# Kernel optimization log

Measured on AMD Instinct MI355X. Metric: run time of the kernel, lower is better.

Reference implementation:

```python
import jax, jax.numpy as jnp
import numpy as np

B, V, T, S, C, NH, H, MULT = 1, 2, 2, 16384, 128, 9, 4, 2
DH = C // H


def _ln(x, g, b):
    m = jnp.mean(x, -1, keepdims=True)
    v = jnp.mean((x - m) ** 2, -1, keepdims=True)
    return (x - m) * jax.lax.rsqrt(v + 1e-5) * g + b


def setup_inputs():
    key = jax.random.key(0)
    ks = jax.random.split(key, 16)
    sc = 0.02
    return {
        "x": jax.random.normal(ks[0], (B, V, T, S, C), jnp.float32),
        "adjc": jax.random.randint(ks[1], (S, NH), 0, S, dtype=jnp.int32),
        "mask": jax.random.bernoulli(ks[2], 0.1, (B, V, T, S)),
        "ln1_g": jnp.ones((C,), jnp.float32),
        "ln1_b": jnp.zeros((C,), jnp.float32),
        "Wq": sc * jax.random.normal(ks[3], (C, C), jnp.float32),
        "Wkv": sc * jax.random.normal(ks[4], (C, 2 * C), jnp.float32),
        "b_kv": jnp.zeros((2 * C,), jnp.float32),
        "W_nh": sc * jax.random.normal(ks[5], (NH, NH), jnp.float32),
        "W_ao": sc * jax.random.normal(ks[6], (C, C), jnp.float32),
        "ln2_g": jnp.ones((C,), jnp.float32),
        "ln2_b": jnp.zeros((C,), jnp.float32),
        "W1": sc * jax.random.normal(ks[7], (C, MULT * C), jnp.float32),
        "b1": jnp.zeros((MULT * C,), jnp.float32),
        "W2": sc * jax.random.normal(ks[8], (MULT * C, C), jnp.float32),
        "b2": jnp.zeros((C,), jnp.float32),
        "gamma": 0.1 * jnp.ones((C,), jnp.float32),
        "Wout": sc * jax.random.normal(ks[9], (C, C), jnp.float32),
    }


def reference(x, adjc, mask, ln1_g, ln1_b, Wq, Wkv, b_kv, W_nh, W_ao,
              ln2_g, ln2_b, W1, b1, W2, b2, gamma, Wout):
    # 1. per-zoom embedding layer (LayerNorm, identity linear)
    xe = _ln(x, ln1_g, ln1_b)  # [b,v,t,s,c]
    # 2. query projection, q_len = 1 per grid cell
    q = jnp.einsum("bvtsc,cd->bvtsd", xe, Wq)
    # 3. neighborhood gather (grid_layer.get_nh) + fused KV projection
    kv_nh = xe[:, :, :, adjc, :]                       # [b,v,t,s,nh,c]
    kv = jnp.einsum("bvtsnc,cd->bvtsnd", kv_nh, Wkv) + b_kv  # [b,v,t,s,nh,2c]
    # factorized nh-mixing with residual skip (skip_dims=[True,...])
    kv = kv + jnp.einsum("bvtsnd,nm->bvtsmd", kv, W_nh)
    # 4. gathered neighbor mask (True = masked out)
    m_nh = mask[:, :, :, adjc]                          # [b,v,t,s,nh]
    # 5. multi-head cross attention, q_len=1, kv_len=nh
    k, v = jnp.split(kv, 2, axis=-1)                    # each [b,v,t,s,nh,c]
    qh = q.reshape(B, V, T, S, H, DH)
    kh = k.reshape(B, V, T, S, NH, H, DH)
    vh = v.reshape(B, V, T, S, NH, H, DH)
    scores = jnp.einsum("bvtshd,bvtsnhd->bvtshn", qh, kh) / jnp.sqrt(
        jnp.asarray(DH, qh.dtype))
    scores = jnp.where(m_nh[:, :, :, :, None, :], -1e9, scores)
    attn = jax.nn.softmax(scores, axis=-1)
    o = jnp.einsum("bvtshn,bvtsnhd->bvtshd", attn, vh).reshape(B, V, T, S, C)
    o = jnp.einsum("bvtsc,cd->bvtsd", o, W_ao)
    # 6. residual insert
    x = x + o
    # 7. MLP block with layer-scale gamma
    xm = _ln(x, ln2_g, ln2_b)
    h = jax.nn.gelu(jnp.einsum("bvtsc,cd->bvtsd", xm, W1) + b1)
    x = x + gamma * (jnp.einsum("bvtsd,dc->bvtsc", h, W2) + b2)
    # 8. output layer
    return jnp.einsum("bvtsc,cd->bvtsd", x, Wout)
```

## Files before the change

### kernel.cpp

```cpp
#include <hip/hip_runtime.h>
#include <math.h>

namespace {

typedef float f32x4 __attribute__((ext_vector_type(4)));
typedef short s16x8 __attribute__((ext_vector_type(8)));

constexpr int C_   = 128;
constexpr int S_   = 16384;
constexpr int NTOK = 65536;

__device__ __forceinline__ unsigned short f2bf(float f) {
    unsigned int u = __float_as_uint(f);
    unsigned int r = (u + 0x7FFFu + ((u >> 16) & 1u)) >> 16;
    return (unsigned short)r;
}
__device__ __forceinline__ float bf2f(unsigned short h) {
    return __uint_as_float(((unsigned int)h) << 16);
}
__device__ __forceinline__ float gelu_tanh(float v) {
    const float k0 = 0.7978845608028654f;
    float u = k0 * (v + 0.044715f * v * v * v);
    float au = fabsf(u);
    float E = __expf(2.0f * au);
    float th = 1.0f - 2.0f / (1.0f + E);
    th = (u < 0.f) ? -th : th;
    return 0.5f * v * (1.0f + th);
}

__global__ __launch_bounds__(256) void prep_weights(
    const float* __restrict__ Wq, const float* __restrict__ Wkv,
    const float* __restrict__ W_ao, const float* __restrict__ W1,
    const float* __restrict__ W2, const float* __restrict__ Wout,
    unsigned short* __restrict__ Wf)
{
    int idx = blockIdx.x * 256 + threadIdx.x;
    if (idx >= 147456) return;
    int seg, off, K, N; const float* src = nullptr;
    if (idx < 49152)       { seg = 0; off = 0;      K = 128; N = 384; }
    else if (idx < 65536)  { seg = 1; off = 49152;  K = 128; N = 128; src = W_ao; }
    else if (idx < 98304)  { seg = 2; off = 65536;  K = 128; N = 256; src = W1; }
    else if (idx < 131072) { seg = 3; off = 98304;  K = 256; N = 128; src = W2; }
    else                   { seg = 4; off = 131072; K = 128; N = 128; src = Wout; }
    int local = idx - off;
    int j    = local & 7;
    int lane = (local >> 3) & 63;
    int tl   = local >> 9;
    int KB   = K >> 5;
    int kb   = tl % KB;
    int nt   = tl / KB;
    int k    = kb * 32 + ((lane >> 4) << 3) + j;
    int col  = (nt << 4) + (lane & 15);
    float v;
    if (seg == 0) v = (col < 128) ? Wq[k * 128 + col] : Wkv[k * 256 + (col - 128)];
    else          v = src[k * N + col];
    Wf[idx] = f2bf(v);
}

__global__ __launch_bounds__(256, 2) void qkv_kernel(
    const float* __restrict__ x,
    const float* __restrict__ ln1_g, const float* __restrict__ ln1_b,
    const unsigned short* __restrict__ Wf,
    const float* __restrict__ b_kv,
    float* qout, unsigned short* __restrict__ kout,
    unsigned short* __restrict__ vout)
{
    __shared__ unsigned short xet[64 * 128];
    const int tile = blockIdx.x;
    const int t = threadIdx.x;

    {
        const int row = t >> 2;
        const int q4  = t & 3;
        const int tok = tile * 64 + row;
        const float* xr = x + (size_t)tok * C_ + q4 * 32;
        float v[32];
        float s0 = 0.f, s1 = 0.f;
        #pragma unroll
        for (int i = 0; i < 32; i += 4) {
            float4 f = *(const float4*)(xr + i);
            v[i] = f.x; v[i+1] = f.y; v[i+2] = f.z; v[i+3] = f.w;
            s0 += f.x + f.y + f.z + f.w;
            s1 += f.x*f.x + f.y*f.y + f.z*f.z + f.w*f.w;
        }
        s0 += __shfl_xor(s0, 1, 64); s1 += __shfl_xor(s1, 1, 64);
        s0 += __shfl_xor(s0, 2, 64); s1 += __shfl_xor(s1, 2, 64);
        const float mean = s0 * (1.0f / C_);
        const float var  = s1 * (1.0f / C_) - mean * mean;
        const float inv  = rsqrtf(var + 1e-5f);
        #pragma unroll
        for (int jj = 0; jj < 4; ++jj) {
            unsigned short tmp[8];
            #pragma unroll
            for (int j = 0; j < 8; ++j) {
                int k = q4 * 32 + jj * 8 + j;
                tmp[j] = f2bf((v[jj*8 + j] - mean) * inv * ln1_g[k] + ln1_b[k]);
            }
            int byte = row * 256 + (q4 * 32 + jj * 8) * 2;
            byte ^= (row & 7) << 4;
            *(s16x8*)((char*)xet + byte) = *(const s16x8*)tmp;
        }
    }
    __syncthreads();

    const int w = t >> 6, l = t & 63;
    const int arow = (w << 4) + (l & 15);
    s16x8 af[4];
    #pragma unroll
    for (int kb = 0; kb < 4; ++kb) {
        int byte = arow * 256 + (kb * 32 + ((l >> 4) << 3)) * 2;
        byte ^= (arow & 7) << 4;
        af[kb] = *(const s16x8*)((const char*)xet + byte);
    }
    f32x4 acc[24];
    #pragma unroll
    for (int nt = 0; nt < 24; ++nt) acc[nt] = (f32x4){0.f, 0.f, 0.f, 0.f};
    #pragma unroll
    for (int nt = 0; nt < 24; ++nt) {
        #pragma unroll
        for (int kb = 0; kb < 4; ++kb) {
            s16x8 bf = *(const s16x8*)(Wf + (size_t)((nt * 4 + kb) * 64 + l) * 8);
            acc[nt] = __builtin_amdgcn_mfma_f32_16x16x32_bf16(af[kb], bf, acc[nt], 0, 0, 0);
        }
    }
    const int r0 = (l >> 4) << 2;
    const int colb = l & 15;
    #pragma unroll
    for (int nt = 0; nt < 8; ++nt) {
        const int col = nt * 16 + colb;
        #pragma unroll
        for (int reg = 0; reg < 4; ++reg) {
            const size_t tokr = (size_t)tile * 64 + (w << 4) + r0 + reg;
            qout[tokr * 128 + col] = acc[nt][reg];
        }
    }
    #pragma unroll
    for (int i = 0; i < 8; ++i) {
        const int ch = i * 16 + colb;
        const float bk = b_kv[ch];
        const float bv = b_kv[ch + 128];
        #pragma unroll
        for (int reg = 0; reg < 4; ++reg) {
            const size_t tokr = (size_t)tile * 64 + (w << 4) + r0 + reg;
            kout[tokr * 128 + ch] = f2bf(acc[8 + i][reg] + bk);
            vout[tokr * 128 + ch] = f2bf(acc[16 + i][reg] + bv);
        }
    }
}

__global__ __launch_bounds__(256, 5) void attn_kernel(
    const int* __restrict__ adjc, const unsigned char* __restrict__ mask,
    const float* __restrict__ wnh,
    const float* __restrict__ qbuf,
    const unsigned short* __restrict__ kbuf,
    const unsigned short* __restrict__ vbuf,
    unsigned short* __restrict__ obuf)
{
    __shared__ unsigned int sidx[32][9];

    const int d   = blockIdx.x;
    const int xcd = d & 7, dj = d >> 3;
    const int bid = (xcd >> 1) * 512 + dj * 2 + (xcd & 1);
    const size_t base = (size_t)bid * 32;
    const int s0  = (int)(base & (S_ - 1));
    const int bvt = (int)(base >> 14);
    const int t = threadIdx.x;

    for (int i = t; i < 288; i += 256) {
        int r = i / 9, n = i - r * 9;
        int nb = adjc[(s0 + r) * 9 + n];
        unsigned int gi = (unsigned int)(bvt * S_ + nb);
        sidx[r][n] = gi | (mask[gi] ? 0x80000000u : 0u);
    }
    __syncthreads();

    const int w = t >> 6, l = t & 63;
    const int g = l >> 3, j = l & 7;
    const int r = w * 8 + g;
    const size_t tok = base + r;

    float q[16];
    {
        const float4* qp = (const float4*)(qbuf + tok * 128 + j * 16);
        #pragma unroll
        for (int i = 0; i < 4; ++i) {
            float4 f = qp[i];
            q[4*i] = f.x; q[4*i+1] = f.y; q[4*i+2] = f.z; q[4*i+3] = f.w;
        }
    }
    unsigned int gm[9];
    #pragma unroll
    for (int n = 0; n < 9; ++n) gm[n] = sidx[r][n];

    float sp[9];
    #pragma unroll
    for (int n = 0; n < 9; ++n) {
        const s16x8* kp = (const s16x8*)(kbuf +
            (size_t)(gm[n] & 0x7fffffffu) * 128 + j * 16);
        s16x8 k0 = kp[0], k1 = kp[1];
        float a = 0.f;
        #pragma unroll
        for (int i = 0; i < 8; ++i) a += q[i]     * bf2f((unsigned short)k0[i]);
        #pragma unroll
        for (int i = 0; i < 8; ++i) a += q[8 + i] * bf2f((unsigned short)k1[i]);
        sp[n] = a;
    }
    #pragma unroll
    for (int n = 0; n < 9; ++n) sp[n] += __shfl_xor(sp[n], 1, 64);

    float S[9];
    #pragma unroll
    for (int m = 0; m < 9; ++m) {
        float a = sp[m];
        #pragma unroll
        for (int n = 0; n < 9; ++n) a += sp[n] * wnh[n * 9 + m];
        a *= 0.17677669529663687f;
        S[m] = (gm[m] & 0x80000000u) ? -1e9f : a;
    }
    float mx = S[0];
    #pragma unroll
    for (int m = 1; m < 9; ++m) mx = fmaxf(mx, S[m]);
    float e[9], se = 0.f;
    #pragma unroll
    for (int m = 0; m < 9; ++m) { e[m] = __expf(S[m] - mx); se += e[m]; }
    const float inv = 1.f / se;

    float ap[9];
    #pragma unroll
    for (int n = 0; n < 9; ++n) {
        float a = e[n];
        #pragma unroll
        for (int m = 0; m < 9; ++m) a += wnh[n * 9 + m] * e[m];
        ap[n] = a * inv;
    }

    float o[16];
    #pragma unroll
    for (int i = 0; i < 16; ++i) o[i] = 0.f;
    #pragma unroll
    for (int n = 0; n < 9; ++n) {
        const s16x8* vp = (const s16x8*)(vbuf +
            (size_t)(gm[n] & 0x7fffffffu) * 128 + j * 16);
        s16x8 v0 = vp[0], v1 = vp[1];
        const float a = ap[n];
        #pragma unroll
        for (int i = 0; i < 8; ++i) o[i]     += a * bf2f((unsigned short)v0[i]);
        #pragma unroll
        for (int i = 0; i < 8; ++i) o[8 + i] += a * bf2f((unsigned short)v1[i]);
    }
    unsigned short tmp[16];
    #pragma unroll
    for (int i = 0; i < 16; ++i) tmp[i] = f2bf(o[i]);
    s16x8* op = (s16x8*)(obuf + tok * 256 + j * 16);
    op[0] = *(const s16x8*)tmp;
    op[1] = *(const s16x8*)(tmp + 8);
}

__global__ __launch_bounds__(256, 2) void mlp_kernel(
    const float* __restrict__ x,
    const unsigned short* obuf,
    const unsigned short* __restrict__ Wao_f, const unsigned short* __restrict__ W1f,
    const unsigned short* __restrict__ W2f, const unsigned short* __restrict__ Woutf,
    const float* __restrict__ ln2_g, const float* __restrict__ ln2_b,
    const float* __restrict__ b1, const float* __restrict__ b2,
    const float* __restrict__ gamma,
    float* outp)
{
    __shared__ unsigned short act[8192];
    __shared__ float sred[2][32][2];
    const int tile = blockIdx.x;
    const int t = threadIdx.x;
    const int w = t >> 6, l = t & 63;
    const int wr = w >> 1, wc = w & 1;
    const int arow = (wr << 4) + (l & 15);
    const int crow0 = (wr << 4) + ((l >> 4) << 2);
    const int colb = l & 15;
    const size_t base = (size_t)tile * 32;

    s16x8 af[4];
    #pragma unroll
    for (int kb = 0; kb < 4; ++kb)
        af[kb] = *(const s16x8*)(obuf + (base + arow) * 256 + kb * 32 + ((l >> 4) << 3));
    f32x4 acc1[4];
    #pragma unroll
    for (int nt = 0; nt < 4; ++nt) acc1[nt] = (f32x4){0.f, 0.f, 0.f, 0.f};
    #pragma unroll
    for (int nt = 0; nt < 4; ++nt) {
        const int ntg = wc * 4 + nt;
        #pragma unroll
        for (int kb = 0; kb < 4; ++kb) {
            s16x8 bf = *(const s16x8*)(Wao_f + (size_t)((ntg * 4 + kb) * 64 + l) * 8);
            acc1[nt] = __builtin_amdgcn_mfma_f32_16x16x32_bf16(af[kb], bf, acc1[nt], 0, 0, 0);
        }
    }

    float x1v[4][4];
    float ss[4] = {0.f, 0.f, 0.f, 0.f}, s2[4] = {0.f, 0.f, 0.f, 0.f};
    #pragma unroll
    for (int nt = 0; nt < 4; ++nt) {
        const int col = wc * 64 + nt * 16 + colb;
        #pragma unroll
        for (int reg = 0; reg < 4; ++reg) {
            const size_t tokr = base + crow0 + reg;
            float xv = x[tokr * 128 + col] + acc1[nt][reg];
            x1v[nt][reg] = xv;
            ss[reg] += xv;
            s2[reg] += xv * xv;
        }
    }
    #pragma unroll
    for (int off = 1; off < 16; off <<= 1) {
        #pragma unroll
        for (int reg = 0; reg < 4; ++reg) {
            ss[reg] += __shfl_xor(ss[reg], off, 64);
            s2[reg] += __shfl_xor(s2[reg], off, 64);
        }
    }
    if (colb == 0) {
        #pragma unroll
        for (int reg = 0; reg < 4; ++reg) {
            sred[wc][crow0 + reg][0] = ss[reg];
            sred[wc][crow0 + reg][1] = s2[reg];
        }
    }
    __syncthreads();
    float mean[4], inv[4];
    #pragma unroll
    for (int reg = 0; reg < 4; ++reg) {
        const int row = crow0 + reg;
        float sum = sred[0][row][0] + sred[1][row][0];
        float sq  = sred[0][row][1] + sred[1][row][1];
        mean[reg] = sum * (1.0f / 128.f);
        float var = sq * (1.0f / 128.f) - mean[reg] * mean[reg];
        inv[reg] = rsqrtf(var + 1e-5f);
    }
    #pragma unroll
    for (int nt = 0; nt < 4; ++nt) {
        const int col = wc * 64 + nt * 16 + colb;
        const float lg = ln2_g[col], lb = ln2_b[col];
        #pragma unroll
        for (int reg = 0; reg < 4; ++reg) {
            const int lrow = crow0 + reg;
            float xm = (x1v[nt][reg] - mean[reg]) * inv[reg] * lg + lb;
            int byte = lrow * 256 + col * 2;
            byte ^= (lrow & 7) << 4;
            *(unsigned short*)((char*)act + byte) = f2bf(xm);
        }
    }
    __syncthreads();

    #pragma unroll
    for (int kb = 0; kb < 4; ++kb) {
        int byte = arow * 256 + (kb * 32 + ((l >> 4) << 3)) * 2;
        byte ^= (arow & 7) << 4;
        af[kb] = *(const s16x8*)((const char*)act + byte);
    }
    f32x4 acc2[8];
    #pragma unroll
    for (int nt = 0; nt < 8; ++nt) acc2[nt] = (f32x4){0.f, 0.f, 0.f, 0.f};
    #pragma unroll
    for (int nt = 0; nt < 8; ++nt) {
        const int ntg = wc * 8 + nt;
        #pragma unroll
        for (int kb = 0; kb < 4; ++kb) {
            s16x8 bf = *(const s16x8*)(W1f + (size_t)((ntg * 4 + kb) * 64 + l) * 8);
            acc2[nt] = __builtin_amdgcn_mfma_f32_16x16x32_bf16(af[kb], bf, acc2[nt], 0, 0, 0);
        }
    }
    __syncthreads();
    #pragma unroll
    for (int nt = 0; nt < 8; ++nt) {
        const int col2 = wc * 128 + nt * 16 + colb;
        const float bb = b1[col2];
        #pragma unroll
        for (int reg = 0; reg < 4; ++reg) {
            const int lrow = crow0 + reg;
            float hv = gelu_tanh(acc2[nt][reg] + bb);
            int byte = lrow * 512 + col2 * 2;
            byte ^= (lrow & 7) << 4;
            *(unsigned short*)((char*)act + byte) = f2bf(hv);
        }
    }
    __syncthreads();

    f32x4 acc3[4];
    #pragma unroll
    for (int nt = 0; nt < 4; ++nt) acc3[nt] = (f32x4){0.f, 0.f, 0.f, 0.f};
    #pragma unroll
    for (int kb = 0; kb < 8; ++kb) {
        int byte = arow * 512 + (kb * 32 + ((l >> 4) << 3)) * 2;
        byte ^= (arow & 7) << 4;
        s16x8 hf = *(const s16x8*)((const char*)act + byte);
        #pragma unroll
        for (int nt = 0; nt < 4; ++nt) {
            const int ntg = wc * 4 + nt;
            s16x8 bf = *(const s16x8*)(W2f + (size_t)((ntg * 8 + kb) * 64 + l) * 8);
            acc3[nt] = __builtin_amdgcn_mfma_f32_16x16x32_bf16(hf, bf, acc3[nt], 0, 0, 0);
        }
    }
    __syncthreads();
    #pragma unroll
    for (int nt = 0; nt < 4; ++nt) {
        const int col = wc * 64 + nt * 16 + colb;
        const float gm = gamma[col], bb = b2[col];
        #pragma unroll
        for (int reg = 0; reg < 4; ++reg) {
            const int lrow = crow0 + reg;
            float y = x1v[nt][reg] + gm * (acc3[nt][reg] + bb);
            int byte = lrow * 256 + col * 2;
            byte ^= (lrow & 7) << 4;
            *(unsigned short*)((char*)act + byte) = f2bf(y);
        }
    }
    __syncthreads();

    #pragma unroll
    for (int kb = 0; kb < 4; ++kb) {
        int byte = arow * 256 + (kb * 32 + ((l >> 4) << 3)) * 2;
        byte ^= (arow & 7) << 4;
        af[kb] = *(const s16x8*)((const char*)act + byte);
    }
    f32x4 acc4[4];
    #pragma unroll
    for (int nt = 0; nt < 4; ++nt) acc4[nt] = (f32x4){0.f, 0.f, 0.f, 0.f};
    #pragma unroll
    for (int nt = 0; nt < 4; ++nt) {
        const int ntg = wc * 4 + nt;
        #pragma unroll
        for (int kb = 0; kb < 4; ++kb) {
            s16x8 bf = *(const s16x8*)(Woutf + (size_t)((ntg * 4 + kb) * 64 + l) * 8);
            acc4[nt] = __builtin_amdgcn_mfma_f32_16x16x32_bf16(af[kb], bf, acc4[nt], 0, 0, 0);
        }
    }
    #pragma unroll
    for (int nt = 0; nt < 4; ++nt) {
        const int col = wc * 64 + nt * 16 + colb;
        #pragma unroll
        for (int reg = 0; reg < 4; ++reg) {
            const size_t tokr = base + crow0 + reg;
            outp[tokr * 128 + col] = acc4[nt][reg];
        }
    }
}

}

extern "C" void kernel_launch(void* const* d_in, const int* in_sizes, int n_in,
                              void* d_out, int out_size, void* d_ws, size_t ws_size,
                              hipStream_t stream) {
    const float* x     = (const float*)d_in[0];
    const int*   adjc  = (const int*)d_in[1];
    const unsigned char* mask = (const unsigned char*)d_in[2];
    const float* ln1_g = (const float*)d_in[3];
    const float* ln1_b = (const float*)d_in[4];
    const float* Wq    = (const float*)d_in[5];
    const float* Wkv   = (const float*)d_in[6];
    const float* b_kv  = (const float*)d_in[7];
    const float* W_nh  = (const float*)d_in[8];
    const float* W_ao  = (const float*)d_in[9];
    const float* ln2_g = (const float*)d_in[10];
    const float* ln2_b = (const float*)d_in[11];
    const float* W1    = (const float*)d_in[12];
    const float* b1    = (const float*)d_in[13];
    const float* W2    = (const float*)d_in[14];
    const float* b2    = (const float*)d_in[15];
    const float* gamma = (const float*)d_in[16];
    const float* Wout  = (const float*)d_in[17];

    unsigned short* kbuf = (unsigned short*)d_ws;
    unsigned short* vbuf = kbuf + (size_t)NTOK * 128;
    unsigned short* Wf   = vbuf + (size_t)NTOK * 128;
    unsigned short* Wao_f  = Wf + 49152;
    unsigned short* W1f    = Wf + 65536;
    unsigned short* W2f    = Wf + 98304;
    unsigned short* Woutf  = Wf + 131072;

    float*          qbuf = (float*)d_out;
    unsigned short* obuf = (unsigned short*)d_out;

    prep_weights<<<576, 256, 0, stream>>>(Wq, Wkv, W_ao, W1, W2, Wout, Wf);
    qkv_kernel<<<NTOK / 64, 256, 0, stream>>>(x, ln1_g, ln1_b, Wf, b_kv,
                                              qbuf, kbuf, vbuf);
    attn_kernel<<<NTOK / 32, 256, 0, stream>>>(adjc, mask, W_nh,
                                               qbuf, kbuf, vbuf, obuf);
    mlp_kernel<<<NTOK / 32, 256, 0, stream>>>(x, obuf, Wao_f, W1f, W2f, Woutf,
                                              ln2_g, ln2_b, b1, b2, gamma,
                                              (float*)d_out);
}
```

Baseline: 157.8 us.

## Fuse neighborhood attention into MLP kernel via shared-memory handoff

Merges the attention kernel and the MLP kernel into one launch. Each block first computes the gathered-neighbor attention output for its 32 tokens and writes it in bf16 to a swizzled LDS tile. The Wao/MLP stage then reads its MFMA operands from that tile instead of a global intermediate buffer. This removes the global write and re-read of the attention output and one kernel launch. In exchange, the latency-bound gather phase now runs at the MLP kernel's lower occupancy bound (2 blocks instead of 5), and an extra barrier is needed before the LDS tile is reused.

Result: faster. 134.2 us (-15.0%).

```diff
diff --git a/kernel.cpp b/kernel.cpp
--- a/kernel.cpp
+++ b/kernel.cpp
@@ -148,117 +148,13 @@
     }
 }
 
-__global__ __launch_bounds__(256, 5) void attn_kernel(
+__global__ __launch_bounds__(256, 2) void attn_mlp_kernel(
+    const float* __restrict__ x,
     const int* __restrict__ adjc, const unsigned char* __restrict__ mask,
     const float* __restrict__ wnh,
     const float* __restrict__ qbuf,
     const unsigned short* __restrict__ kbuf,
     const unsigned short* __restrict__ vbuf,
-    unsigned short* __restrict__ obuf)
-{
-    __shared__ unsigned int sidx[32][9];
-
-    const int d   = blockIdx.x;
-    const int xcd = d & 7, dj = d >> 3;
-    const int bid = (xcd >> 1) * 512 + dj * 2 + (xcd & 1);
-    const size_t base = (size_t)bid * 32;
-    const int s0  = (int)(base & (S_ - 1));
-    const int bvt = (int)(base >> 14);
-    const int t = threadIdx.x;
-
-    for (int i = t; i < 288; i += 256) {
-        int r = i / 9, n = i - r * 9;
-        int nb = adjc[(s0 + r) * 9 + n];
-        unsigned int gi = (unsigned int)(bvt * S_ + nb);
-        sidx[r][n] = gi | (mask[gi] ? 0x80000000u : 0u);
-    }
-    __syncthreads();
-
-    const int w = t >> 6, l = t & 63;
-    const int g = l >> 3, j = l & 7;
-    const int r = w * 8 + g;
-    const size_t tok = base + r;
-
-    float q[16];
-    {
-        const float4* qp = (const float4*)(qbuf + tok * 128 + j * 16);
-        #pragma unroll
-        for (int i = 0; i < 4; ++i) {
-            float4 f = qp[i];
-            q[4*i] = f.x; q[4*i+1] = f.y; q[4*i+2] = f.z; q[4*i+3] = f.w;
-        }
-    }
-    unsigned int gm[9];
-    #pragma unroll
-    for (int n = 0; n < 9; ++n) gm[n] = sidx[r][n];
-
-    float sp[9];
-    #pragma unroll
-    for (int n = 0; n < 9; ++n) {
-        const s16x8* kp = (const s16x8*)(kbuf +
-            (size_t)(gm[n] & 0x7fffffffu) * 128 + j * 16);
-        s16x8 k0 = kp[0], k1 = kp[1];
-        float a = 0.f;
-        #pragma unroll
-        for (int i = 0; i < 8; ++i) a += q[i]     * bf2f((unsigned short)k0[i]);
-        #pragma unroll
-        for (int i = 0; i < 8; ++i) a += q[8 + i] * bf2f((unsigned short)k1[i]);
-        sp[n] = a;
-    }
-    #pragma unroll
-    for (int n = 0; n < 9; ++n) sp[n] += __shfl_xor(sp[n], 1, 64);
-
-    float S[9];
-    #pragma unroll
-    for (int m = 0; m < 9; ++m) {
-        float a = sp[m];
-        #pragma unroll
-        for (int n = 0; n < 9; ++n) a += sp[n] * wnh[n * 9 + m];
-        a *= 0.17677669529663687f;
-        S[m] = (gm[m] & 0x80000000u) ? -1e9f : a;
-    }
-    float mx = S[0];
-    #pragma unroll
-    for (int m = 1; m < 9; ++m) mx = fmaxf(mx, S[m]);
-    float e[9], se = 0.f;
-    #pragma unroll
-    for (int m = 0; m < 9; ++m) { e[m] = __expf(S[m] - mx); se += e[m]; }
-    const float inv = 1.f / se;
-
-    float ap[9];
-    #pragma unroll
-    for (int n = 0; n < 9; ++n) {
-        float a = e[n];
-        #pragma unroll
-        for (int m = 0; m < 9; ++m) a += wnh[n * 9 + m] * e[m];
-        ap[n] = a * inv;
-    }
-
-    float o[16];
-    #pragma unroll
-    for (int i = 0; i < 16; ++i) o[i] = 0.f;
-    #pragma unroll
-    for (int n = 0; n < 9; ++n) {
-        const s16x8* vp = (const s16x8*)(vbuf +
-            (size_t)(gm[n] & 0x7fffffffu) * 128 + j * 16);
-        s16x8 v0 = vp[0], v1 = vp[1];
-        const float a = ap[n];
-        #pragma unroll
-        for (int i = 0; i < 8; ++i) o[i]     += a * bf2f((unsigned short)v0[i]);
-        #pragma unroll
-        for (int i = 0; i < 8; ++i) o[8 + i] += a * bf2f((unsigned short)v1[i]);
-    }
-    unsigned short tmp[16];
-    #pragma unroll
-    for (int i = 0; i < 16; ++i) tmp[i] = f2bf(o[i]);
-    s16x8* op = (s16x8*)(obuf + tok * 256 + j * 16);
-    op[0] = *(const s16x8*)tmp;
-    op[1] = *(const s16x8*)(tmp + 8);
-}
-
-__global__ __launch_bounds__(256, 2) void mlp_kernel(
-    const float* __restrict__ x,
-    const unsigned short* obuf,
     const unsigned short* __restrict__ Wao_f, const unsigned short* __restrict__ W1f,
     const unsigned short* __restrict__ W2f, const unsigned short* __restrict__ Woutf,
     const float* __restrict__ ln2_g, const float* __restrict__ ln2_b,
@@ -268,19 +164,120 @@
 {
     __shared__ unsigned short act[8192];
     __shared__ float sred[2][32][2];
-    const int tile = blockIdx.x;
+    __shared__ unsigned int sidx[32][9];
+
+    const int d   = blockIdx.x;
+    const int xcd = d & 7, dj = d >> 3;
+    const int bid = (xcd >> 1) * 512 + dj * 2 + (xcd & 1);
+    const size_t base = (size_t)bid * 32;
+    const int s0  = (int)(base & (S_ - 1));
+    const int bvt = (int)(base >> 14);
     const int t = threadIdx.x;
+
+    for (int i = t; i < 288; i += 256) {
+        int r = i / 9, n = i - r * 9;
+        int nb = adjc[(s0 + r) * 9 + n];
+        unsigned int gi = (unsigned int)(bvt * S_ + nb);
+        sidx[r][n] = gi | (mask[gi] ? 0x80000000u : 0u);
+    }
+    __syncthreads();
+
+    {
+        const int r = t >> 3, j = t & 7;
+        const size_t tok = base + r;
+
+        float q[16];
+        {
+            const float4* qp = (const float4*)(qbuf + tok * 128 + j * 16);
+            #pragma unroll
+            for (int i = 0; i < 4; ++i) {
+                float4 f = qp[i];
+                q[4*i] = f.x; q[4*i+1] = f.y; q[4*i+2] = f.z; q[4*i+3] = f.w;
+            }
+        }
+        unsigned int gm[9];
+        #pragma unroll
+        for (int n = 0; n < 9; ++n) gm[n] = sidx[r][n];
+
+        float sp[9];
+        #pragma unroll
+        for (int n = 0; n < 9; ++n) {
+            const s16x8* kp = (const s16x8*)(kbuf +
+                (size_t)(gm[n] & 0x7fffffffu) * 128 + j * 16);
+            s16x8 k0 = kp[0], k1 = kp[1];
+            float a = 0.f;
+            #pragma unroll
+            for (int i = 0; i < 8; ++i) a += q[i]     * bf2f((unsigned short)k0[i]);
+            #pragma unroll
+            for (int i = 0; i < 8; ++i) a += q[8 + i] * bf2f((unsigned short)k1[i]);
+            sp[n] = a;
+        }
+        #pragma unroll
+        for (int n = 0; n < 9; ++n) sp[n] += __shfl_xor(sp[n], 1, 64);
+
+        float S[9];
+        #pragma unroll
+        for (int m = 0; m < 9; ++m) {
+            float a = sp[m];
+            #pragma unroll
+            for (int n = 0; n < 9; ++n) a += sp[n] * wnh[n * 9 + m];
+            a *= 0.17677669529663687f;
+            S[m] = (gm[m] & 0x80000000u) ? -1e9f : a;
+        }
+        float mx = S[0];
+        #pragma unroll
+        for (int m = 1; m < 9; ++m) mx = fmaxf(mx, S[m]);
+        float e[9], se = 0.f;
+        #pragma unroll
+        for (int m = 0; m < 9; ++m) { e[m] = __expf(S[m] - mx); se += e[m]; }
+        const float inv = 1.f / se;
+
+        float ap[9];
+        #pragma unroll
+        for (int n = 0; n < 9; ++n) {
+            float a = e[n];
+            #pragma unroll
+            for (int m = 0; m < 9; ++m) a += wnh[n * 9 + m] * e[m];
+            ap[n] = a * inv;
+        }
+
+        float o[16];
+        #pragma unroll
+        for (int i = 0; i < 16; ++i) o[i] = 0.f;
+        #pragma unroll
+        for (int n = 0; n < 9; ++n) {
+            const s16x8* vp = (const s16x8*)(vbuf +
+                (size_t)(gm[n] & 0x7fffffffu) * 128 + j * 16);
+            s16x8 v0 = vp[0], v1 = vp[1];
+            const float a = ap[n];
+            #pragma unroll
+            for (int i = 0; i < 8; ++i) o[i]     += a * bf2f((unsigned short)v0[i]);
+            #pragma unroll
+            for (int i = 0; i < 8; ++i) o[8 + i] += a * bf2f((unsigned short)v1[i]);
+        }
+        unsigned short tmp[16];
+        #pragma unroll
+        for (int i = 0; i < 16; ++i) tmp[i] = f2bf(o[i]);
+        int b0 = (r * 256 + j * 32) ^ ((r & 7) << 4);
+        int b1_ = (r * 256 + j * 32 + 16) ^ ((r & 7) << 4);
+        *(s16x8*)((char*)act + b0)  = *(const s16x8*)tmp;
+        *(s16x8*)((char*)act + b1_) = *(const s16x8*)(tmp + 8);
+    }
+    __syncthreads();
+
     const int w = t >> 6, l = t & 63;
     const int wr = w >> 1, wc = w & 1;
     const int arow = (wr << 4) + (l & 15);
     const int crow0 = (wr << 4) + ((l >> 4) << 2);
     const int colb = l & 15;
-    const size_t base = (size_t)tile * 32;
 
     s16x8 af[4];
     #pragma unroll
-    for (int kb = 0; kb < 4; ++kb)
-        af[kb] = *(const s16x8*)(obuf + (base + arow) * 256 + kb * 32 + ((l >> 4) << 3));
+    for (int kb = 0; kb < 4; ++kb) {
+        int byte = arow * 256 + (kb * 32 + ((l >> 4) << 3)) * 2;
+        byte ^= (arow & 7) << 4;
+        af[kb] = *(const s16x8*)((const char*)act + byte);
+    }
     f32x4 acc1[4];
     #pragma unroll
     for (int nt = 0; nt < 4; ++nt) acc1[nt] = (f32x4){0.f, 0.f, 0.f, 0.f};
@@ -334,6 +331,7 @@
         float var = sq * (1.0f / 128.f) - mean[reg] * mean[reg];
         inv[reg] = rsqrtf(var + 1e-5f);
     }
+    __syncthreads();
     #pragma unroll
     for (int nt = 0; nt < 4; ++nt) {
         const int col = wc * 64 + nt * 16 + colb;
@@ -475,15 +473,14 @@
     unsigned short* W2f    = Wf + 98304;
     unsigned short* Woutf  = Wf + 131072;
 
-    float*          qbuf = (float*)d_out;
-    unsigned short* obuf = (unsigned short*)d_out;
+    float* qbuf = (float*)d_out;
 
     prep_weights<<<576, 256, 0, stream>>>(Wq, Wkv, W_ao, W1, W2, Wout, Wf);
     qkv_kernel<<<NTOK / 64, 256, 0, stream>>>(x, ln1_g, ln1_b, Wf, b_kv,
                                               qbuf, kbuf, vbuf);
-    attn_kernel<<<NTOK / 32, 256, 0, stream>>>(adjc, mask, W_nh,
-                                               qbuf, kbuf, vbuf, obuf);
-    mlp_kernel<<<NTOK / 32, 256, 0, stream>>>(x, obuf, Wao_f, W1f, W2f, Woutf,
-                                              ln2_g, ln2_b, b1, b2, gamma,
-                                              (float*)d_out);
-}
+    attn_mlp_kernel<<<NTOK / 32, 256, 0, stream>>>(x, adjc, mask, W_nh,
+                                                   qbuf, kbuf, vbuf,
+                                                   Wao_f, W1f, W2f, Woutf,
+                                                   ln2_g, ln2_b, b1, b2, gamma,
+                                                   (float*)d_out);
+}
```
